# Kernel tuning notes

Hardware: AMD Instinct MI355X
Metric: run time of the kernel (lower is better)

## Reference

```python
import jax, jax.numpy as jnp
import numpy as np

VOCAB = 50000
D = 512          # sru output_dim (input_size == hidden_size)
L = 2            # n_sru_layers
B = 8
T = 2048


def setup_inputs() -> dict:
    key = jax.random.key(0)
    ks = jax.random.split(key, 6)
    ids = jax.random.randint(ks[0], (B, T), 0, VOCAB)
    # ragged valid lengths -> mask True = real token, False = pad
    lens = jax.random.randint(ks[1], (B,), T // 2, T + 1)
    mask = jnp.arange(T)[None, :] < lens[:, None]
    emb = jax.random.normal(ks[2], (VOCAB, D), jnp.float32) * 0.02
    # per-layer SRU params: W projects to (x_tilde, f, r); v = peephole weight_c; b = gate biases
    Ws = jax.random.normal(ks[3], (L, D, 3 * D), jnp.float32) / np.sqrt(D)
    vs = jax.random.normal(ks[4], (L, 2 * D), jnp.float32) * 0.1
    bs = jnp.zeros((L, 2 * D), jnp.float32)
    return {"ids": ids, "mask": mask, "emb": emb, "Ws": Ws, "vs": vs, "bs": bs}


def _sru_layer(x, W, v, b, pad):
    # x: [T,B,D] time-major, pad: [T,B] True where padded
    Tn, Bn, d = x.shape
    U = jnp.einsum('tbd,de->tbe', x, W).reshape(Tn, Bn, 3, d)
    vf, vr = v[:d], v[d:]
    bf, br = b[:d], b[d:]

    def step(c, inp):
        xt, u, m = inp                      # xt:[B,d] u:[B,3,d] m:[B]
        u0, u1, u2 = u[:, 0], u[:, 1], u[:, 2]
        f = jax.nn.sigmoid(u1 + vf * c + bf)
        r = jax.nn.sigmoid(u2 + vr * c + br)
        c_new = f * c + (1.0 - f) * u0
        h = r * jnp.tanh(c_new) + (1.0 - r) * xt   # highway (input==hidden)
        m_ = m[:, None]
        c_out = jnp.where(m_, c, c_new)     # padded steps keep state
        h = jnp.where(m_, 0.0, h)           # and emit zeros
        return c_out, h

    c0 = jnp.zeros((Bn, d), x.dtype)
    _, hs = jax.lax.scan(step, c0, (x, U, pad))
    return hs


def reference(ids, mask, emb, Ws, vs, bs):
    x = emb[ids]                     # char embedder -> [B,T,D]
    x = jnp.transpose(x, (1, 0, 2))  # [T,B,D]
    pad = (~mask).T                  # inverted mask, transposed -> [T,B]
    for l in range(Ws.shape[0]):
        x = _sru_layer(x, Ws[l], vs[l], bs[l], pad)
    return jnp.transpose(x, (1, 0, 2))  # back to [B,T,D]
```

## Files before the change

kernel.cpp:

```cpp
#include <hip/hip_runtime.h>
#include <hip/hip_bf16.h>

#define D 512
#define L_LAYERS 2
#define BATCH 8
#define TT 2048
#define N3 1536
#define REC 4096

typedef __attribute__((ext_vector_type(8))) short short8;
typedef __attribute__((ext_vector_type(4))) float floatx4;

#if __has_builtin(__builtin_amdgcn_exp2f)
#define EXP2F(x) __builtin_amdgcn_exp2f(x)
#else
#define EXP2F(x) exp2f(x)
#endif
#if __has_builtin(__builtin_amdgcn_rcpf)
#define RCPF(x) __builtin_amdgcn_rcpf(x)
#else
#define RCPF(x) (1.0f / (x))
#endif

__device__ __forceinline__ unsigned short f2bf(float f) {
  unsigned u = __builtin_bit_cast(unsigned, f);
  u += 0x7FFFu + ((u >> 16) & 1u);
  return (unsigned short)(u >> 16);
}

__global__ __launch_bounds__(128) void embed_kernel(const int* __restrict__ ids,
                                                    const float* __restrict__ emb,
                                                    unsigned short* __restrict__ xa) {
  int bt = blockIdx.x;
  int b = bt >> 11;
  int t = bt & 2047;
  int id = ids[bt];
  int d = threadIdx.x << 2;
  const float4 v = *(const float4*)(emb + (size_t)id * D + d);
  ushort4 w;
  w.x = f2bf(v.x); w.y = f2bf(v.y); w.z = f2bf(v.z); w.w = f2bf(v.w);
  *(ushort4*)(xa + ((size_t)t * BATCH + b) * D + d) = w;
}

__global__ __launch_bounds__(256) void wconv_kernel(const float* __restrict__ Ws,
                                                    unsigned short* __restrict__ Wt,
                                                    const void* __restrict__ maskp,
                                                    int* __restrict__ lenb) {
  if (blockIdx.x == 0 && threadIdx.x >= 248) {
    int b = threadIdx.x - 248;
    int w0 = *(const int*)maskp;
    int mode = (w0 == 1) ? 0 : ((w0 == 0x01010101) ? 1 : 2);
    int lo = 0, hi = TT;
    while (lo < hi) {
      int mid = (lo + hi) >> 1;
      int idx = b * TT + mid;
      bool mm = (mode == 0) ? (((const int*)maskp)[idx] != 0)
              : (mode == 1) ? (((const unsigned char*)maskp)[idx] != 0)
                            : (((const float*)maskp)[idx] != 0.f);
      if (mm) lo = mid + 1; else hi = mid;
    }
    lenb[b] = lo;
  }
  int idx = blockIdx.x * 256 + threadIdx.x;
  if (idx >= L_LAYERS * D * N3) return;
  int n = idx % N3;
  int k = (idx / N3) % D;
  int l = idx / (N3 * D);
  Wt[((size_t)l * N3 + n) * D + k] = f2bf(Ws[idx]);
}

__global__ __launch_bounds__(512) void gemm_kernel(const unsigned short* __restrict__ A,
                                                   const unsigned short* __restrict__ Bt,
                                                   unsigned* __restrict__ Ua32,
                                                   unsigned short* __restrict__ Uc16) {
  constexpr int K = D;
  __shared__ __align__(16) unsigned short As[128 * 32];
  __shared__ __align__(16) unsigned short Bs[384 * 32];
  int tid = threadIdx.x;
  int lane = tid & 63;
  int wave = tid >> 6;
  int bi = blockIdx.x;
  int xcd = bi & 7;
  int j = bi >> 3;
  int bm = xcd * 16 + (j >> 2);
  int dc0 = (j & 3) * 128;
  int m0 = bm * 128;
  int wm = (wave & 1) * 64;
  int w2 = wave >> 1;
  int q = lane >> 4, r16 = lane & 15;

  int arow = tid >> 2;
  int aoff = (tid & 3) * 8;
  int nsrc[3];
#pragma unroll
  for (int i = 0; i < 3; ++i) {
    int c = arow + i * 128;
    int g = c >> 4;
    int p = g % 3;
    int dcol = (g / 3) * 16 + (c & 15);
    nsrc[i] = dc0 + dcol + p * 512;
  }
  const unsigned short* asrc = A + (size_t)(m0 + arow) * K + aoff;

  floatx4 acc[4][6] = {};

  for (int k0 = 0; k0 < K; k0 += 32) {
    __builtin_amdgcn_global_load_lds(
        (const __attribute__((address_space(1))) unsigned int*)(asrc + k0),
        (__attribute__((address_space(3))) unsigned int*)(As + tid * 8), 16, 0, 0);
#pragma unroll
    for (int i = 0; i < 3; ++i) {
      __builtin_amdgcn_global_load_lds(
          (const __attribute__((address_space(1))) unsigned int*)(Bt + (size_t)nsrc[i] * K + k0 + aoff),
          (__attribute__((address_space(3))) unsigned int*)(Bs + i * 4096 + tid * 8), 16, 0, 0);
    }
    __syncthreads();
    short8 af[4], bfr[6];
#pragma unroll
    for (int i = 0; i < 4; ++i)
      af[i] = *(const short8*)&As[(wm + i * 16 + r16) * 32 + q * 8];
#pragma unroll
    for (int i = 0; i < 6; ++i)
      bfr[i] = *(const short8*)&Bs[(w2 * 96 + i * 16 + r16) * 32 + q * 8];
#pragma unroll
    for (int mi = 0; mi < 4; ++mi)
#pragma unroll
      for (int ni = 0; ni < 6; ++ni)
        acc[mi][ni] = __builtin_amdgcn_mfma_f32_16x16x32_bf16(af[mi], bfr[ni], acc[mi][ni], 0, 0, 0);
    __syncthreads();
  }

#pragma unroll
  for (int mi = 0; mi < 4; ++mi)
#pragma unroll
    for (int half = 0; half < 2; ++half) {
      int dcol = dc0 + w2 * 32 + half * 16 + r16;
#pragma unroll
      for (int i = 0; i < 4; ++i) {
        int m = m0 + wm + mi * 16 + q * 4 + i;
        size_t rec = (size_t)m * D + dcol;
        unsigned ua = (unsigned)f2bf(acc[mi][half * 3 + 0][i]) |
                      ((unsigned)f2bf(acc[mi][half * 3 + 1][i]) << 16);
        Ua32[rec] = ua;
        Uc16[rec] = f2bf(acc[mi][half * 3 + 2][i]);
      }
    }
}

__global__ __launch_bounds__(64) void cchain_kernel(unsigned* __restrict__ Uac,
                                                    const float* __restrict__ vsl,
                                                    const float* __restrict__ bsl,
                                                    const int* __restrict__ lenb) {
  int tid = threadIdx.x;
  int ch = blockIdx.x * 64 + tid;
  int b = ch >> 9;
  int d = ch & 511;
  int len = lenb[b];
  const float NL2E = -1.4426950408889634f;
  float vfe = NL2E * vsl[d];
  float cbf = NL2E * bsl[d];
  const unsigned* pa = Uac + ch;
  float* pc = (float*)Uac + ch;
  int nact = (len + 31) >> 5;

  unsigned uA[32], uB[32];

#define CLOAD(k, u)                                         \
  _Pragma("unroll") for (int j = 0; j < 32; ++j)            \
      u[j] = pa[(size_t)((k) * 32 + j) * REC];

#define CCOMP(k, u)                                         \
  _Pragma("unroll") for (int j = 0; j < 32; ++j) {          \
    unsigned a = u[j];                                      \
    float u0 = __builtin_bit_cast(float, a << 16);          \
    float u1f = __builtin_bit_cast(float, a & 0xFFFF0000u); \
    float k1 = fmaf(u1f, NL2E, cbf);                        \
    float a2 = fmaf(vfe, c, k1);                            \
    float e = EXP2F(a2);                                    \
    float inv = RCPF(e + 1.f);                              \
    c = fmaf(c - u0, inv, u0);                              \
    pc[(size_t)((k) * 32 + j) * REC] = c;                   \
  }

  CLOAD(0, uA);
  float c = 0.f;
  int k = 0;
  for (;;) {
    if (k + 1 < nact) CLOAD(k + 1, uB);
    CCOMP(k, uA);
    if (++k >= nact) break;
    if (k + 1 < nact) CLOAD(k + 1, uA);
    CCOMP(k, uB);
    if (++k >= nact) break;
  }
#undef CLOAD
#undef CCOMP
}

template <bool LAST>
__global__ __launch_bounds__(256) void hpost_kernel(const unsigned short* __restrict__ Uc,
                                                    const unsigned short* __restrict__ Xin,
                                                    const float4* __restrict__ cq,
                                                    const float* __restrict__ vsl,
                                                    const float* __restrict__ bsl,
                                                    const int* __restrict__ lenb,
                                                    unsigned short* __restrict__ Hout,
                                                    float* __restrict__ Out) {
  int idx = blockIdx.x * 256 + threadIdx.x;
  int t = idx >> 10;
  int q = idx & 1023;
  int rec0 = q << 2;
  int b = rec0 >> 9;
  int d = rec0 & 511;
  int len = lenb[b];
  ushort4 uv = *(const ushort4*)(Uc + (size_t)idx * 4);
  ushort4 xv = *(const ushort4*)(Xin + (size_t)idx * 4);
  float4 ct = cq[idx];
  float4 cp = (t > 0) ? cq[idx - 1024] : make_float4(0.f, 0.f, 0.f, 0.f);
  float4 vr4 = *(const float4*)(vsl + D + d);
  float4 br4 = *(const float4*)(bsl + D + d);
  const float NL2E = -1.4426950408889634f;
  const float L2E2 = 2.8853900817779268f;
  unsigned uu[4] = {uv.x, uv.y, uv.z, uv.w};
  unsigned xx[4] = {xv.x, xv.y, xv.z, xv.w};
  float cta[4] = {ct.x, ct.y, ct.z, ct.w};
  float cpa[4] = {cp.x, cp.y, cp.z, cp.w};
  float vra[4] = {vr4.x, vr4.y, vr4.z, vr4.w};
  float bra[4] = {br4.x, br4.y, br4.z, br4.w};
  bool act = t < len;
  float h[4];
#pragma unroll
  for (int j = 0; j < 4; ++j) {
    float u2 = __builtin_bit_cast(float, uu[j] << 16);
    float xf = __builtin_bit_cast(float, xx[j] << 16);
    float k2 = fmaf(u2, NL2E, NL2E * bra[j]);
    float a2 = fmaf(NL2E * vra[j], cpa[j], k2);
    float r = RCPF(EXP2F(a2) + 1.f);
    float et = EXP2F(cta[j] * L2E2);
    float th = fmaf(-2.f, RCPF(et + 1.f), 1.f);
    float hv = fmaf(r, th - xf, xf);
    h[j] = act ? hv : 0.f;
  }
  if (LAST) {
    *(float4*)(Out + ((size_t)b * TT + t) * D + d) = make_float4(h[0], h[1], h[2], h[3]);
  } else {
    ushort4 o; o.x = f2bf(h[0]); o.y = f2bf(h[1]); o.z = f2bf(h[2]); o.w = f2bf(h[3]);
    *(ushort4*)(Hout + (size_t)idx * 4) = o;
  }
}

extern "C" void kernel_launch(void* const* d_in, const int* in_sizes, int n_in,
                              void* d_out, int out_size, void* d_ws, size_t ws_size,
                              hipStream_t stream) {
  const int* ids = (const int*)d_in[0];
  const void* mask = d_in[1];
  const float* emb = (const float*)d_in[2];
  const float* Ws = (const float*)d_in[3];
  const float* vs = (const float*)d_in[4];
  const float* bs = (const float*)d_in[5];
  float* out = (float*)d_out;

  char* ws = (char*)d_ws;
  unsigned short* Ua = (unsigned short*)ws;
  unsigned short* Uc = Ua + (size_t)TT * REC * 2;
  unsigned short* xa = Uc + (size_t)TT * REC;
  unsigned short* xb = xa + (size_t)TT * REC;
  unsigned short* Wt = xb + (size_t)TT * REC;
  int* lenb = (int*)(Wt + (size_t)L_LAYERS * D * N3);

  embed_kernel<<<BATCH * TT, 128, 0, stream>>>(ids, emb, xa);
  wconv_kernel<<<(L_LAYERS * D * N3 + 255) / 256, 256, 0, stream>>>(Ws, Wt, mask, lenb);

  gemm_kernel<<<512, 512, 0, stream>>>(xa, Wt, (unsigned*)Ua, Uc);
  cchain_kernel<<<64, 64, 0, stream>>>((unsigned*)Ua, vs, bs, lenb);
  hpost_kernel<false><<<8192, 256, 0, stream>>>(Uc, xa, (const float4*)Ua,
                                                vs, bs, lenb, xb, nullptr);
  gemm_kernel<<<512, 512, 0, stream>>>(xb, Wt + (size_t)N3 * D, (unsigned*)Ua, Uc);
  cchain_kernel<<<64, 64, 0, stream>>>((unsigned*)Ua, vs + 2 * D, bs + 2 * D, lenb);
  hpost_kernel<true><<<8192, 256, 0, stream>>>(Uc, xb, (const float4*)Ua,
                                               vs + 2 * D, bs + 2 * D, lenb, nullptr, out);
}
```

Baseline: 474.0 us.

## Fuse the c-recurrence chain and h post-processing into one warp-specialized kernel

Merges the sequential c-chain kernel and the parallel h-output kernel into one kernel. One wavefront computes the c recurrence into a double-buffered shared-memory tile of 32 timesteps, and a second wavefront consumes the previous tile to compute r, tanh and the highway output. Padded tail steps are zero-filled. This removes the fp32 c write-back to global memory, the separate h-kernel launch and its re-read of c. The cost is that the h work now runs on only 64 blocks of 2 waves, synchronised every 32 steps with __syncthreads, instead of being spread across the whole GPU.

```diff
diff --git a/kernel.cpp b/kernel.cpp
--- a/kernel.cpp
+++ b/kernel.cpp
@@ -147,29 +147,42 @@
     }
 }
 
-__global__ __launch_bounds__(64) void cchain_kernel(unsigned* __restrict__ Uac,
-                                                    const float* __restrict__ vsl,
-                                                    const float* __restrict__ bsl,
-                                                    const int* __restrict__ lenb) {
+template <bool LAST>
+__global__ __launch_bounds__(128) void chainh_kernel(const unsigned* __restrict__ Ua,
+                                                     const unsigned short* __restrict__ Uc,
+                                                     const unsigned short* __restrict__ Xin,
+                                                     const float* __restrict__ vsl,
+                                                     const float* __restrict__ bsl,
+                                                     const int* __restrict__ lenb,
+                                                     unsigned short* __restrict__ Hout,
+                                                     float* __restrict__ Out) {
+  __shared__ float cbuf[2][32 * 64];
   int tid = threadIdx.x;
-  int ch = blockIdx.x * 64 + tid;
+  int lane = tid & 63;
+  int w = tid >> 6;
+  int ch = blockIdx.x * 64 + lane;
   int b = ch >> 9;
   int d = ch & 511;
   int len = lenb[b];
+  int nact = (len + 31) >> 5;
   const float NL2E = -1.4426950408889634f;
-  float vfe = NL2E * vsl[d];
-  float cbf = NL2E * bsl[d];
-  const unsigned* pa = Uac + ch;
-  float* pc = (float*)Uac + ch;
-  int nact = (len + 31) >> 5;
-
-  unsigned uA[32], uB[32];
+  const float L2E2 = 2.8853900817779268f;
+  unsigned short* ph = Hout + ch;
+  float* po = Out + (size_t)b * TT * D + d;
+
+  if (w == 0) {
+    float vfe = NL2E * vsl[d];
+    float cbf = NL2E * bsl[d];
+    const unsigned* pa = Ua + ch;
+    float* cb0 = &cbuf[0][0];
+    float* cb1 = &cbuf[1][0];
+    unsigned uA[32], uB[32];
 
 #define CLOAD(k, u)                                         \
   _Pragma("unroll") for (int j = 0; j < 32; ++j)            \
       u[j] = pa[(size_t)((k) * 32 + j) * REC];
 
-#define CCOMP(k, u)                                         \
+#define CCOMP(k, u, cb)                                     \
   _Pragma("unroll") for (int j = 0; j < 32; ++j) {          \
     unsigned a = u[j];                                      \
     float u0 = __builtin_bit_cast(float, a << 16);          \
@@ -179,73 +192,68 @@
     float e = EXP2F(a2);                                    \
     float inv = RCPF(e + 1.f);                              \
     c = fmaf(c - u0, inv, u0);                              \
-    pc[(size_t)((k) * 32 + j) * REC] = c;                   \
-  }
-
-  CLOAD(0, uA);
-  float c = 0.f;
-  int k = 0;
-  for (;;) {
-    if (k + 1 < nact) CLOAD(k + 1, uB);
-    CCOMP(k, uA);
-    if (++k >= nact) break;
-    if (k + 1 < nact) CLOAD(k + 1, uA);
-    CCOMP(k, uB);
-    if (++k >= nact) break;
-  }
+    cb[j * 64 + lane] = c;                                  \
+  }
+
+    CLOAD(0, uA);
+    float c = 0.f;
+    int p = 0;
+    for (;;) {
+      if (p + 1 < nact) CLOAD(p + 1, uB);
+      CCOMP(p, uA, cb0);
+      __syncthreads();
+      if (++p >= nact) break;
+      if (p + 1 < nact) CLOAD(p + 1, uA);
+      CCOMP(p, uB, cb1);
+      __syncthreads();
+      if (++p >= nact) break;
+    }
 #undef CLOAD
 #undef CCOMP
-}
-
-template <bool LAST>
-__global__ __launch_bounds__(256) void hpost_kernel(const unsigned short* __restrict__ Uc,
-                                                    const unsigned short* __restrict__ Xin,
-                                                    const float4* __restrict__ cq,
-                                                    const float* __restrict__ vsl,
-                                                    const float* __restrict__ bsl,
-                                                    const int* __restrict__ lenb,
-                                                    unsigned short* __restrict__ Hout,
-                                                    float* __restrict__ Out) {
-  int idx = blockIdx.x * 256 + threadIdx.x;
-  int t = idx >> 10;
-  int q = idx & 1023;
-  int rec0 = q << 2;
-  int b = rec0 >> 9;
-  int d = rec0 & 511;
-  int len = lenb[b];
-  ushort4 uv = *(const ushort4*)(Uc + (size_t)idx * 4);
-  ushort4 xv = *(const ushort4*)(Xin + (size_t)idx * 4);
-  float4 ct = cq[idx];
-  float4 cp = (t > 0) ? cq[idx - 1024] : make_float4(0.f, 0.f, 0.f, 0.f);
-  float4 vr4 = *(const float4*)(vsl + D + d);
-  float4 br4 = *(const float4*)(bsl + D + d);
-  const float NL2E = -1.4426950408889634f;
-  const float L2E2 = 2.8853900817779268f;
-  unsigned uu[4] = {uv.x, uv.y, uv.z, uv.w};
-  unsigned xx[4] = {xv.x, xv.y, xv.z, xv.w};
-  float cta[4] = {ct.x, ct.y, ct.z, ct.w};
-  float cpa[4] = {cp.x, cp.y, cp.z, cp.w};
-  float vra[4] = {vr4.x, vr4.y, vr4.z, vr4.w};
-  float bra[4] = {br4.x, br4.y, br4.z, br4.w};
-  bool act = t < len;
-  float h[4];
-#pragma unroll
-  for (int j = 0; j < 4; ++j) {
-    float u2 = __builtin_bit_cast(float, uu[j] << 16);
-    float xf = __builtin_bit_cast(float, xx[j] << 16);
-    float k2 = fmaf(u2, NL2E, NL2E * bra[j]);
-    float a2 = fmaf(NL2E * vra[j], cpa[j], k2);
-    float r = RCPF(EXP2F(a2) + 1.f);
-    float et = EXP2F(cta[j] * L2E2);
-    float th = fmaf(-2.f, RCPF(et + 1.f), 1.f);
-    float hv = fmaf(r, th - xf, xf);
-    h[j] = act ? hv : 0.f;
-  }
-  if (LAST) {
-    *(float4*)(Out + ((size_t)b * TT + t) * D + d) = make_float4(h[0], h[1], h[2], h[3]);
   } else {
-    ushort4 o; o.x = f2bf(h[0]); o.y = f2bf(h[1]); o.z = f2bf(h[2]); o.w = f2bf(h[3]);
-    *(ushort4*)(Hout + (size_t)idx * 4) = o;
+    float vre = NL2E * vsl[D + d];
+    float cbr = NL2E * bsl[D + d];
+    const unsigned short* pu = Uc + ch;
+    const unsigned short* px = Xin + ch;
+    float cprev = 0.f;
+
+#define HPROC(q)                                                \
+  {                                                             \
+    int t0h = (q) * 32;                                         \
+    const float* cb = &cbuf[(q) & 1][0];                        \
+    unsigned short ucr[32], xxr[32];                            \
+    _Pragma("unroll") for (int j = 0; j < 32; ++j) {            \
+      ucr[j] = pu[(size_t)(t0h + j) * REC];                     \
+      xxr[j] = px[(size_t)(t0h + j) * REC];                     \
+    }                                                           \
+    _Pragma("unroll") for (int j = 0; j < 32; ++j) {            \
+      int t = t0h + j;                                          \
+      float ct = cb[j * 64 + lane];                             \
+      float u2 = __builtin_bit_cast(float, (unsigned)ucr[j] << 16); \
+      float xf = __builtin_bit_cast(float, (unsigned)xxr[j] << 16); \
+      float a2r = fmaf(vre, cprev, fmaf(u2, NL2E, cbr));        \
+      float r = RCPF(EXP2F(a2r) + 1.f);                         \
+      float et = EXP2F(ct * L2E2);                              \
+      float th = fmaf(-2.f, RCPF(et + 1.f), 1.f);               \
+      float hv = fmaf(r, th - xf, xf);                          \
+      hv = (t < len) ? hv : 0.f;                                \
+      if (LAST) po[(size_t)t * D] = hv;                         \
+      else      ph[(size_t)t * REC] = f2bf(hv);                 \
+      cprev = ct;                                               \
+    }                                                           \
+  }
+
+    for (int p = 0; p < nact; ++p) {
+      if (p > 0) HPROC(p - 1);
+      __syncthreads();
+    }
+    HPROC(nact - 1);
+#undef HPROC
+  }
+
+  for (int t = nact * 32 + w; t < TT; t += 2) {
+    if (LAST) po[(size_t)t * D] = 0.f;
+    else      ph[(size_t)t * REC] = 0;
   }
 }
 
@@ -272,11 +280,9 @@
   wconv_kernel<<<(L_LAYERS * D * N3 + 255) / 256, 256, 0, stream>>>(Ws, Wt, mask, lenb);
 
   gemm_kernel<<<512, 512, 0, stream>>>(xa, Wt, (unsigned*)Ua, Uc);
-  cchain_kernel<<<64, 64, 0, stream>>>((unsigned*)Ua, vs, bs, lenb);
-  hpost_kernel<false><<<8192, 256, 0, stream>>>(Uc, xa, (const float4*)Ua,
-                                                vs, bs, lenb, xb, nullptr);
+  chainh_kernel<false><<<64, 128, 0, stream>>>((const unsigned*)Ua, Uc, xa,
+                                               vs, bs, lenb, xb, nullptr);
   gemm_kernel<<<512, 512, 0, stream>>>(xb, Wt + (size_t)N3 * D, (unsigned*)Ua, Uc);
-  cchain_kernel<<<64, 64, 0, stream>>>((unsigned*)Ua, vs + 2 * D, bs + 2 * D, lenb);
-  hpost_kernel<true><<<8192, 256, 0, stream>>>(Uc, xb, (const float4*)Ua,
-                                               vs + 2 * D, bs + 2 * D, lenb, nullptr, out);
-}
+  chainh_kernel<true><<<64, 128, 0, stream>>>((const unsigned*)Ua, Uc, xb,
+                                              vs + 2 * D, bs + 2 * D, lenb, nullptr, out);
+}
```

Result: slower. 672.8 us (+42.0%).
